# Kernel tuning notes

Measured on AMD Instinct MI355X. Metric: run time of the kernel, lower is better.

The kernel has to match this reference:

```python
import jax, jax.numpy as jnp
import numpy as np

N_NODES = 50000
N_EDGES = 800000
LATENT = 32
NODE_IN = 6
EDGE_IN = 3
STEPS = 10
OUT_DIM = 1
NEG_SLOPE = 0.01
LN_EPS = 1e-5


def _leaky(x):
    return jnp.where(x >= 0, x, NEG_SLOPE * x)


def _layernorm(x, scale, bias):
    mu = jnp.mean(x, axis=-1, keepdims=True)
    var = jnp.mean(jnp.square(x - mu), axis=-1, keepdims=True)
    return (x - mu) * jax.lax.rsqrt(var + LN_EPS) * scale + bias


def setup_inputs() -> dict:
    key = jax.random.key(0)
    ks = jax.random.split(key, 24)
    g = lambda i, shape, fan_in: (jax.random.normal(ks[i], shape, jnp.float32)
                                  / np.sqrt(fan_in)).astype(jnp.float32)
    return {
        "x": jax.random.normal(ks[0], (N_NODES, NODE_IN), jnp.float32),
        "edge_attr": jax.random.normal(ks[1], (N_EDGES, EDGE_IN), jnp.float32),
        "senders": jax.random.randint(ks[2], (N_EDGES,), 0, N_NODES, jnp.int32),
        "receivers": jax.random.randint(ks[3], (N_EDGES,), 0, N_NODES, jnp.int32),
        # input embedders (Linear + LeakyReLU)
        "node_enc_W": g(4, (NODE_IN, LATENT), NODE_IN),
        "node_enc_b": jnp.zeros((LATENT,), jnp.float32),
        "edge_enc_W": g(5, (EDGE_IN, LATENT), EDGE_IN),
        "edge_enc_b": jnp.zeros((LATENT,), jnp.float32),
        # per-step edge update: concat(e, x_src, x_dst) -> latent
        "edge_W": g(6, (STEPS, 3 * LATENT, LATENT), 3 * LATENT),
        "edge_b": jnp.zeros((STEPS, LATENT), jnp.float32),
        "edge_ln_scale": jnp.ones((STEPS, LATENT), jnp.float32),
        "edge_ln_bias": jnp.zeros((STEPS, LATENT), jnp.float32),
        # per-step node update: concat(x, agg) -> latent
        "node_W": g(7, (STEPS, 2 * LATENT, LATENT), 2 * LATENT),
        "node_b": jnp.zeros((STEPS, LATENT), jnp.float32),
        "node_ln_scale": jnp.ones((STEPS, LATENT), jnp.float32),
        "node_ln_bias": jnp.zeros((STEPS, LATENT), jnp.float32),
        # decoder
        "dec_W1": g(8, (LATENT, LATENT), LATENT),
        "dec_b1": jnp.zeros((LATENT,), jnp.float32),
        "dec_W2": g(9, (LATENT, OUT_DIM), LATENT),
        "dec_b2": jnp.zeros((OUT_DIM,), jnp.float32),
    }


def _forward(x, edge_attr, senders, receivers,
             node_enc_W, node_enc_b, edge_enc_W, edge_enc_b,
             edge_W, edge_b, edge_ln_scale, edge_ln_bias,
             node_W, node_b, node_ln_scale, node_ln_bias,
             dec_W1, dec_b1, dec_W2, dec_b2):
    n = x.shape[0]
    # encode raw features into latent space
    h = _leaky(x @ node_enc_W + node_enc_b)            # [N, L]
    e = _leaky(edge_attr @ edge_enc_W + edge_enc_b)    # [E, L]
    # receiver in-degree for scatter-mean (constant across steps)
    cnt = jax.ops.segment_sum(jnp.ones((e.shape[0],), e.dtype), receivers,
                              num_segments=n)
    inv_cnt = (1.0 / jnp.maximum(cnt, 1.0))[:, None]   # [N, 1]

    def step(carry, p):
        h, e = carry
        eW, eb, es, ebi, nW, nb, ns, nbi = p
        # edge update: MLP(concat(e, h_src, h_dst)) + inner LN + residual
        m = jnp.concatenate([e, h[senders], h[receivers]], axis=-1)  # [E, 3L]
        m = _layernorm(_leaky(m @ eW + eb), es, ebi)
        e = e + m
        # node update: scatter-mean over receivers, MLP + inner LN + residual
        agg = jax.ops.segment_sum(e, receivers, num_segments=n) * inv_cnt
        u = jnp.concatenate([h, agg], axis=-1)                       # [N, 2L]
        u = _layernorm(_leaky(u @ nW + nb), ns, nbi)
        h = h + u
        return (h, e), None

    (h, e), _ = jax.lax.scan(step, (h, e),
                             (edge_W, edge_b, edge_ln_scale, edge_ln_bias,
                              node_W, node_b, node_ln_scale, node_ln_bias))
    # decoder: Linear -> LeakyReLU -> Linear
    return _leaky(h @ dec_W1 + dec_b1) @ dec_W2 + dec_b2  # [N, 1]


def reference(x, edge_attr, senders, receivers,
              node_enc_W, node_enc_b, edge_enc_W, edge_enc_b,
              edge_W, edge_b, edge_ln_scale, edge_ln_bias,
              node_W, node_b, node_ln_scale, node_ln_bias,
              dec_W1, dec_b1, dec_W2, dec_b2):
    return _forward(x, edge_attr, senders, receivers,
                    node_enc_W, node_enc_b, edge_enc_W, edge_enc_b,
                    edge_W, edge_b, edge_ln_scale, edge_ln_bias,
                    node_W, node_b, node_ln_scale, node_ln_bias,
                    dec_W1, dec_b1, dec_W2, dec_b2)
```

## Files before the change

### kernel.cpp

```cpp
#include <hip/hip_runtime.h>
#include <hip/hip_bf16.h>

#define N_NODES 50000
#define N_EDGES 800000
#define LATENT 32
#define STEPS 10
#define NEG_SLOPE 0.01f
#define LN_EPS 1e-5f
#define N_TILES (N_EDGES / 16)
#define TPW 8
#define TILES_PER_BLOCK 32
#define SCAN_BLK 256
#define SCAN_NBLK ((N_NODES + SCAN_BLK - 1) / SCAN_BLK)
#define STG_STRIDE 36

typedef __attribute__((ext_vector_type(8))) __bf16 bf16x8;
typedef __attribute__((ext_vector_type(4))) __bf16 bf16x4;
typedef __attribute__((ext_vector_type(4))) float f32x4;

__device__ __forceinline__ float leaky(float x) {
    return x >= 0.0f ? x : NEG_SLOPE * x;
}

__device__ __forceinline__ float4 f4fma(float a, float4 b, float4 c) {
    c.x += a * b.x; c.y += a * b.y; c.z += a * b.z; c.w += a * b.w;
    return c;
}

__device__ __forceinline__ bf16x4 pack4(float4 v) {
    bf16x4 o;
    o[0] = (__bf16)v.x; o[1] = (__bf16)v.y; o[2] = (__bf16)v.z; o[3] = (__bf16)v.w;
    return o;
}


__global__ void encode_nodes_kernel(const float* __restrict__ x,
                                    const float* __restrict__ W,
                                    const float* __restrict__ b,
                                    float* __restrict__ h,
                                    __bf16* __restrict__ hbf) {
    __shared__ __align__(16) float Ws[6 * 32];
    __shared__ __align__(16) float bs[32];
    int tid = threadIdx.x;
    if (tid < 192) Ws[tid] = W[tid];
    if (tid < 32) bs[tid] = b[tid];
    __syncthreads();
    int n = blockIdx.x * blockDim.x + tid;
    if (n >= N_NODES) return;
    float xv[6];
#pragma unroll
    for (int k = 0; k < 6; k++) xv[k] = x[(size_t)n * 6 + k];
    float4 acc[8];
#pragma unroll
    for (int q = 0; q < 8; q++) acc[q] = *(const float4*)&bs[q * 4];
#pragma unroll
    for (int k = 0; k < 6; k++) {
#pragma unroll
        for (int q = 0; q < 8; q++) {
            float4 w = *(const float4*)&Ws[k * 32 + q * 4];
            acc[q] = f4fma(xv[k], w, acc[q]);
        }
    }
#pragma unroll
    for (int q = 0; q < 8; q++) {
        float4 o = acc[q];
        o.x = leaky(o.x); o.y = leaky(o.y); o.z = leaky(o.z); o.w = leaky(o.w);
        *(float4*)&h[(size_t)n * 32 + q * 4] = o;
        *(bf16x4*)&hbf[(size_t)n * 32 + q * 4] = pack4(o);
    }
}


__global__ void count_kernel(const int* __restrict__ recv, int* __restrict__ cnt) {
    int i = blockIdx.x * blockDim.x + threadIdx.x;
    if (i < N_EDGES) atomicAdd(&cnt[recv[i]], 1);
}

__global__ void csr_reduce_kernel(const int* __restrict__ cnt, int* __restrict__ partial) {
    __shared__ int sdata[SCAN_BLK];
    int tid = threadIdx.x;
    int idx = blockIdx.x * SCAN_BLK + tid;
    sdata[tid] = (idx < N_NODES) ? cnt[idx] : 0;
    __syncthreads();
#pragma unroll
    for (int off = SCAN_BLK / 2; off > 0; off >>= 1) {
        if (tid < off) sdata[tid] += sdata[tid + off];
        __syncthreads();
    }
    if (tid == 0) partial[blockIdx.x] = sdata[0];
}

__global__ void csr_scan_partials_kernel(int* __restrict__ partial,
                                         int* __restrict__ row_start) {
    __shared__ int sdata[SCAN_BLK];
    int tid = threadIdx.x;
    int v = (tid < SCAN_NBLK) ? partial[tid] : 0;
    sdata[tid] = v;
    __syncthreads();
#pragma unroll
    for (int off = 1; off < SCAN_BLK; off <<= 1) {
        int t = (tid >= off) ? sdata[tid - off] : 0;
        __syncthreads();
        sdata[tid] += t;
        __syncthreads();
    }
    if (tid < SCAN_NBLK) partial[tid] = sdata[tid] - v;
    if (tid == SCAN_BLK - 1) row_start[N_NODES] = sdata[SCAN_BLK - 1];
}

__global__ void csr_apply_kernel(const int* __restrict__ cnt,
                                 const int* __restrict__ partial,
                                 int* __restrict__ row_start,
                                 int* __restrict__ cursor) {
    __shared__ int sdata[SCAN_BLK];
    int tid = threadIdx.x;
    int idx = blockIdx.x * SCAN_BLK + tid;
    int v = (idx < N_NODES) ? cnt[idx] : 0;
    sdata[tid] = v;
    __syncthreads();
#pragma unroll
    for (int off = 1; off < SCAN_BLK; off <<= 1) {
        int t = (tid >= off) ? sdata[tid - off] : 0;
        __syncthreads();
        sdata[tid] += t;
        __syncthreads();
    }
    if (idx < N_NODES) {
        int out = partial[blockIdx.x] + sdata[tid] - v;
        row_start[idx] = out;
        cursor[idx] = out;
    }
}

__global__ void scatter_encode_kernel(const float* __restrict__ ea,
                                      const int* __restrict__ senders,
                                      const int* __restrict__ receivers,
                                      int* __restrict__ cursor,
                                      const float* __restrict__ W,
                                      const float* __restrict__ b,
                                      __bf16* __restrict__ e,
                                      unsigned int* __restrict__ sr_p) {
    __shared__ __align__(16) float Ws[3 * 32];
    __shared__ __align__(16) float bs[32];
    int tid = threadIdx.x;
    if (tid < 96) Ws[tid] = W[tid];
    if (tid < 32) bs[tid] = b[tid];
    __syncthreads();
    int i = blockIdx.x * blockDim.x + tid;
    if (i >= N_EDGES) return;
    int s = senders[i];
    int r = receivers[i];
    float xv[3];
#pragma unroll
    for (int k = 0; k < 3; k++) xv[k] = ea[(size_t)i * 3 + k];
    int pos = atomicAdd(&cursor[r], 1);
    float4 acc[8];
#pragma unroll
    for (int q = 0; q < 8; q++) acc[q] = *(const float4*)&bs[q * 4];
#pragma unroll
    for (int k = 0; k < 3; k++) {
#pragma unroll
        for (int q = 0; q < 8; q++) {
            float4 w = *(const float4*)&Ws[k * 32 + q * 4];
            acc[q] = f4fma(xv[k], w, acc[q]);
        }
    }
    __bf16* er = e + (size_t)pos * 32;
#pragma unroll
    for (int q = 0; q < 4; q++) {
        float4 lo = acc[2 * q], hi = acc[2 * q + 1];
        bf16x8 v;
        v[0] = (__bf16)leaky(lo.x); v[1] = (__bf16)leaky(lo.y);
        v[2] = (__bf16)leaky(lo.z); v[3] = (__bf16)leaky(lo.w);
        v[4] = (__bf16)leaky(hi.x); v[5] = (__bf16)leaky(hi.y);
        v[6] = (__bf16)leaky(hi.z); v[7] = (__bf16)leaky(hi.w);
        *(bf16x8*)(er + q * 8) = v;
    }
    sr_p[pos] = (unsigned int)s | ((unsigned int)r << 16);
}


__global__ __launch_bounds__(256) void edge_mfma_kernel(
    __bf16* __restrict__ e,
    const __bf16* __restrict__ hbf,
    const unsigned int* __restrict__ srp,
    const float* __restrict__ W,
    const float* __restrict__ bias,
    const float* __restrict__ ln_s,
    const float* __restrict__ ln_b) {
    __shared__ __align__(16) float Ws[96 * 32];
    __shared__ __align__(16) float prm[96];
    __shared__ __align__(16) float stg[4][16 * STG_STRIDE];
    int tid = threadIdx.x;
    {
        const float4* Wg = (const float4*)W;
        float4* Wl = (float4*)Ws;
#pragma unroll
        for (int r = 0; r < 3; r++) Wl[tid + r * 256] = Wg[tid + r * 256];
        if (tid < 32) {
            prm[tid] = bias[tid];
            prm[32 + tid] = ln_s[tid];
            prm[64 + tid] = ln_b[tid];
        }
    }
    __syncthreads();

    const int wave = tid >> 6;
    const int lane = tid & 63;
    const int n_ = lane & 15;
    const int quad = lane >> 4;
    const int rr = lane >> 2;
    const int jj = lane & 3;

    bf16x8 bf[3][2];
#pragma unroll
    for (int kc = 0; kc < 3; kc++)
#pragma unroll
        for (int oh = 0; oh < 2; oh++) {
            bf16x8 f;
#pragma unroll
            for (int j = 0; j < 8; j++)
                f[j] = (__bf16)Ws[(kc * 32 + quad * 8 + j) * 32 + oh * 16 + n_];
            bf[kc][oh] = f;
        }
    float bia0 = prm[n_], bia1 = prm[16 + n_];
    float lns8[8], lnb8[8];
#pragma unroll
    for (int i = 0; i < 8; i++) {
        lns8[i] = prm[32 + jj * 8 + i];
        lnb8[i] = prm[64 + jj * 8 + i];
    }

    int tile0 = blockIdx.x * TILES_PER_BLOCK + wave * TPW;
    int ntiles = min(TPW, N_TILES - tile0);
    if (ntiles <= 0) return;
    float* mystg = stg[wave];
    const int ed0 = tile0 * 16 + n_;

    unsigned int sr0 = srp[ed0];
    bf16x8 aE = *(const bf16x8*)&e[(size_t)ed0 * 32 + quad * 8];
    bf16x8 aS = *(const bf16x8*)&hbf[(size_t)(sr0 & 0xFFFFu) * 32 + quad * 8];
    bf16x8 aR = *(const bf16x8*)&hbf[(size_t)(sr0 >> 16) * 32 + quad * 8];
    bf16x8 old = *(const bf16x8*)&e[(size_t)(tile0 * 16 + rr) * 32 + jj * 8];
    unsigned int sr_n = 0;
    if (ntiles > 1) sr_n = srp[ed0 + 16];

    for (int t = 0; t < ntiles; t++) {
        int e0 = (tile0 + t) * 16;

        f32x4 acc[2] = {{0.f, 0.f, 0.f, 0.f}, {0.f, 0.f, 0.f, 0.f}};
#pragma unroll
        for (int oh = 0; oh < 2; oh++) {
            acc[oh] = __builtin_amdgcn_mfma_f32_16x16x32_bf16(aE, bf[0][oh], acc[oh], 0, 0, 0);
            acc[oh] = __builtin_amdgcn_mfma_f32_16x16x32_bf16(aS, bf[1][oh], acc[oh], 0, 0, 0);
            acc[oh] = __builtin_amdgcn_mfma_f32_16x16x32_bf16(aR, bf[2][oh], acc[oh], 0, 0, 0);
        }

        bf16x8 aE_n = aE, aS_n = aS, aR_n = aR, old_n = old;
        if (t + 1 < ntiles) {
            int edn = ed0 + (t + 1) * 16;
            aE_n = *(const bf16x8*)&e[(size_t)edn * 32 + quad * 8];
            aS_n = *(const bf16x8*)&hbf[(size_t)(sr_n & 0xFFFFu) * 32 + quad * 8];
            aR_n = *(const bf16x8*)&hbf[(size_t)(sr_n >> 16) * 32 + quad * 8];
            old_n = *(const bf16x8*)&e[(size_t)(e0 + 16 + rr) * 32 + jj * 8];
            if (t + 2 < ntiles) sr_n = srp[ed0 + (t + 2) * 16];
        }

#pragma unroll
        for (int oh = 0; oh < 2; oh++)
#pragma unroll
            for (int g = 0; g < 4; g++)
                mystg[(quad * 4 + g) * STG_STRIDE + oh * 16 + n_] =
                    leaky(acc[oh][g] + (oh ? bia1 : bia0));
        __builtin_amdgcn_wave_barrier();

        f32x4 va = *(const f32x4*)&mystg[rr * STG_STRIDE + jj * 8];
        f32x4 vb = *(const f32x4*)&mystg[rr * STG_STRIDE + jj * 8 + 4];
        float s1 = va[0] + va[1] + va[2] + va[3] + vb[0] + vb[1] + vb[2] + vb[3];
        float s2 = va[0]*va[0] + va[1]*va[1] + va[2]*va[2] + va[3]*va[3]
                 + vb[0]*vb[0] + vb[1]*vb[1] + vb[2]*vb[2] + vb[3]*vb[3];
        s1 += __shfl_xor(s1, 1);  s2 += __shfl_xor(s2, 1);
        s1 += __shfl_xor(s1, 2);  s2 += __shfl_xor(s2, 2);
        float mu = s1 * (1.0f / 32.0f);
        float var = s2 * (1.0f / 32.0f) - mu * mu;
        float inv = rsqrtf(fmaxf(var, 0.0f) + LN_EPS);

        float v[8] = {va[0], va[1], va[2], va[3], vb[0], vb[1], vb[2], vb[3]};
        bf16x8 outp;
#pragma unroll
        for (int i = 0; i < 8; i++)
            outp[i] = (__bf16)((float)old[i] + (v[i] - mu) * inv * lns8[i] + lnb8[i]);
        *(bf16x8*)&e[(size_t)(e0 + rr) * 32 + jj * 8] = outp;
        __builtin_amdgcn_wave_barrier();

        aE = aE_n; aS = aS_n; aR = aR_n; old = old_n;
    }
}


__global__ void node_kernel(float* __restrict__ h,
                            __bf16* __restrict__ hbf,
                            const __bf16* __restrict__ e,
                            const int* __restrict__ row_start,
                            const float* __restrict__ W,
                            const float* __restrict__ bias,
                            const float* __restrict__ ln_s,
                            const float* __restrict__ ln_b) {
    __shared__ __align__(16) float Ws[64 * 32];
    __shared__ __align__(16) float prm[96];
    int tid = threadIdx.x;
    {
        const float4* Wg = (const float4*)W;
        float4* Wl = (float4*)Ws;
#pragma unroll
        for (int r = 0; r < 2; r++) Wl[tid + r * 256] = Wg[tid + r * 256];
        if (tid < 32) {
            prm[tid] = bias[tid];
            prm[32 + tid] = ln_s[tid];
            prm[64 + tid] = ln_b[tid];
        }
    }
    __syncthreads();
    int n = blockIdx.x * blockDim.x + tid;
    if (n >= N_NODES) return;

    int beg = row_start[n], end = row_start[n + 1];
    float c[64];
#pragma unroll
    for (int q = 0; q < 8; q++) {
        float4 v = *(const float4*)&h[(size_t)n * 32 + q * 4];
        c[q * 4 + 0] = v.x; c[q * 4 + 1] = v.y; c[q * 4 + 2] = v.z; c[q * 4 + 3] = v.w;
    }
    float s[32];
#pragma unroll
    for (int k = 0; k < 32; k++) s[k] = 0.0f;
    for (int j = beg; j < end; j++) {
        const __bf16* er = e + (size_t)j * 32;
#pragma unroll
        for (int q = 0; q < 4; q++) {
            bf16x8 v = *(const bf16x8*)(er + q * 8);
#pragma unroll
            for (int k = 0; k < 8; k++) s[q * 8 + k] += (float)v[k];
        }
    }
    float ic = 1.0f / fmaxf((float)(end - beg), 1.0f);
#pragma unroll
    for (int k = 0; k < 32; k++) c[32 + k] = s[k] * ic;

    float4 acc[8];
#pragma unroll
    for (int q = 0; q < 8; q++) acc[q] = *(const float4*)&prm[q * 4];
#pragma unroll
    for (int k = 0; k < 64; k++) {
#pragma unroll
        for (int q = 0; q < 8; q++) {
            float4 w = *(const float4*)&Ws[k * 32 + q * 4];
            acc[q] = f4fma(c[k], w, acc[q]);
        }
    }
    float m[32];
#pragma unroll
    for (int q = 0; q < 8; q++) {
        m[q * 4 + 0] = leaky(acc[q].x);
        m[q * 4 + 1] = leaky(acc[q].y);
        m[q * 4 + 2] = leaky(acc[q].z);
        m[q * 4 + 3] = leaky(acc[q].w);
    }
    float s1 = 0.0f, s2 = 0.0f;
#pragma unroll
    for (int i = 0; i < 32; i++) { s1 += m[i]; s2 += m[i] * m[i]; }
    float mu = s1 * (1.0f / 32.0f);
    float var = s2 * (1.0f / 32.0f) - mu * mu;
    float inv = rsqrtf(fmaxf(var, 0.0f) + LN_EPS);
#pragma unroll
    for (int q = 0; q < 8; q++) {
        float4 sc = *(const float4*)&prm[32 + q * 4];
        float4 bi = *(const float4*)&prm[64 + q * 4];
        float4 res;
        res.x = c[q * 4 + 0] + (m[q * 4 + 0] - mu) * inv * sc.x + bi.x;
        res.y = c[q * 4 + 1] + (m[q * 4 + 1] - mu) * inv * sc.y + bi.y;
        res.z = c[q * 4 + 2] + (m[q * 4 + 2] - mu) * inv * sc.z + bi.z;
        res.w = c[q * 4 + 3] + (m[q * 4 + 3] - mu) * inv * sc.w + bi.w;
        *(float4*)&h[(size_t)n * 32 + q * 4] = res;
        *(bf16x4*)&hbf[(size_t)n * 32 + q * 4] = pack4(res);
    }
}


__global__ void decoder_kernel(const float* __restrict__ h,
                               const float* __restrict__ W1,
                               const float* __restrict__ b1,
                               const float* __restrict__ W2,
                               const float* __restrict__ b2,
                               float* __restrict__ out) {
    __shared__ __align__(16) float W1s[32 * 32];
    __shared__ __align__(16) float prm[65];
    int tid = threadIdx.x;
    {
        const float4* Wg = (const float4*)W1;
        float4* Wl = (float4*)W1s;
        Wl[tid] = Wg[tid];
        if (tid < 32) { prm[tid] = b1[tid]; prm[32 + tid] = W2[tid]; }
        if (tid == 0) prm[64] = b2[0];
    }
    __syncthreads();
    int n = blockIdx.x * blockDim.x + tid;
    if (n >= N_NODES) return;
    float hv[32];
#pragma unroll
    for (int q = 0; q < 8; q++) {
        float4 v = *(const float4*)&h[(size_t)n * 32 + q * 4];
        hv[q * 4 + 0] = v.x; hv[q * 4 + 1] = v.y; hv[q * 4 + 2] = v.z; hv[q * 4 + 3] = v.w;
    }
    float4 acc[8];
#pragma unroll
    for (int q = 0; q < 8; q++) acc[q] = *(const float4*)&prm[q * 4];
#pragma unroll
    for (int k = 0; k < 32; k++) {
#pragma unroll
        for (int q = 0; q < 8; q++) {
            float4 w = *(const float4*)&W1s[k * 32 + q * 4];
            acc[q] = f4fma(hv[k], w, acc[q]);
        }
    }
    float o = prm[64];
#pragma unroll
    for (int q = 0; q < 8; q++) {
        o += leaky(acc[q].x) * prm[32 + q * 4 + 0];
        o += leaky(acc[q].y) * prm[32 + q * 4 + 1];
        o += leaky(acc[q].z) * prm[32 + q * 4 + 2];
        o += leaky(acc[q].w) * prm[32 + q * 4 + 3];
    }
    out[n] = o;
}


extern "C" void kernel_launch(void* const* d_in, const int* in_sizes, int n_in,
                              void* d_out, int out_size, void* d_ws, size_t ws_size,
                              hipStream_t stream) {
    const float* x          = (const float*)d_in[0];
    const float* edge_attr  = (const float*)d_in[1];
    const int*   senders    = (const int*)d_in[2];
    const int*   receivers  = (const int*)d_in[3];
    const float* node_enc_W = (const float*)d_in[4];
    const float* node_enc_b = (const float*)d_in[5];
    const float* edge_enc_W = (const float*)d_in[6];
    const float* edge_enc_b = (const float*)d_in[7];
    const float* edge_W     = (const float*)d_in[8];
    const float* edge_b     = (const float*)d_in[9];
    const float* edge_ln_s  = (const float*)d_in[10];
    const float* edge_ln_b  = (const float*)d_in[11];
    const float* node_W     = (const float*)d_in[12];
    const float* node_b     = (const float*)d_in[13];
    const float* node_ln_s  = (const float*)d_in[14];
    const float* node_ln_b  = (const float*)d_in[15];
    const float* dec_W1     = (const float*)d_in[16];
    const float* dec_b1     = (const float*)d_in[17];
    const float* dec_W2     = (const float*)d_in[18];
    const float* dec_b2     = (const float*)d_in[19];
    float* out = (float*)d_out;

    char* ws = (char*)d_ws;
    size_t off = 0;
    auto alloc = [&](size_t bytes) -> void* {
        void* p = ws + off;
        off = (off + bytes + 255) & ~(size_t)255;
        return p;
    };
    float*        h         = (float*)alloc((size_t)N_NODES * 32 * 4);
    __bf16*       hbf       = (__bf16*)alloc((size_t)N_NODES * 32 * 2);
    __bf16*       e         = (__bf16*)alloc((size_t)N_EDGES * 32 * 2);
    int*          cnt       = (int*)alloc((size_t)N_NODES * 4);
    int*          row_start = (int*)alloc((size_t)(N_NODES + 1) * 4);
    int*          cursor    = (int*)alloc((size_t)N_NODES * 4);
    unsigned int* sr_p      = (unsigned int*)alloc((size_t)N_EDGES * 4);
    int*          partial   = (int*)alloc((size_t)SCAN_BLK * 4);
    (void)ws_size; (void)in_sizes; (void)n_in; (void)out_size;

    hipMemsetAsync(cnt, 0, (size_t)N_NODES * 4, stream);
    encode_nodes_kernel<<<(N_NODES + 255) / 256, 256, 0, stream>>>(x, node_enc_W, node_enc_b, h, hbf);
    count_kernel<<<(N_EDGES + 255) / 256, 256, 0, stream>>>(receivers, cnt);
    csr_reduce_kernel<<<SCAN_NBLK, SCAN_BLK, 0, stream>>>(cnt, partial);
    csr_scan_partials_kernel<<<1, SCAN_BLK, 0, stream>>>(partial, row_start);
    csr_apply_kernel<<<SCAN_NBLK, SCAN_BLK, 0, stream>>>(cnt, partial, row_start, cursor);
    scatter_encode_kernel<<<(N_EDGES + 255) / 256, 256, 0, stream>>>(
        edge_attr, senders, receivers, cursor, edge_enc_W, edge_enc_b, e, sr_p);

    int edge_blocks = (N_TILES + TILES_PER_BLOCK - 1) / TILES_PER_BLOCK;
    for (int s = 0; s < STEPS; s++) {
        edge_mfma_kernel<<<edge_blocks, 256, 0, stream>>>(
            e, hbf, sr_p,
            edge_W + (size_t)s * 96 * 32, edge_b + s * 32,
            edge_ln_s + s * 32, edge_ln_b + s * 32);
        node_kernel<<<(N_NODES + 255) / 256, 256, 0, stream>>>(
            h, hbf, e, row_start, node_W + (size_t)s * 64 * 32, node_b + s * 32,
            node_ln_s + s * 32, node_ln_b + s * 32);
    }
    decoder_kernel<<<(N_NODES + 255) / 256, 256, 0, stream>>>(h, dec_W1, dec_b1, dec_W2, dec_b2, out);
}
```

Before: 743.8 us.

## Split node update across two lanes per node with shuffle reduction

Each node is now processed by two adjacent threads, each owning half of the feature columns for the gather and half of the K dimension of the 64x32 matvec. Partial accumulators are combined with a shuffle-xor, and each half writes its own 16 output columns. The intent is more threads in flight, fewer registers per thread, and coalesced half-row edge reads, at the cost of one shuffle reduction and a duplicated LayerNorm computation.

```diff
diff --git a/kernel.cpp b/kernel.cpp
--- a/kernel.cpp
+++ b/kernel.cpp
@@ -321,43 +321,62 @@
         }
     }
     __syncthreads();
-    int n = blockIdx.x * blockDim.x + tid;
+    int g = blockIdx.x * blockDim.x + tid;
+    int n = g >> 1, half = g & 1;
     if (n >= N_NODES) return;
 
     int beg = row_start[n], end = row_start[n + 1];
-    float c[64];
+    float ch[16];
+#pragma unroll
+    for (int q = 0; q < 4; q++) {
+        float4 v = *(const float4*)&h[(size_t)n * 32 + half * 16 + q * 4];
+        ch[q * 4 + 0] = v.x; ch[q * 4 + 1] = v.y; ch[q * 4 + 2] = v.z; ch[q * 4 + 3] = v.w;
+    }
+    float s[16];
+#pragma unroll
+    for (int k = 0; k < 16; k++) s[k] = 0.0f;
+    for (int j = beg; j < end; j++) {
+        const __bf16* er = e + (size_t)j * 32 + half * 16;
+        bf16x8 v0 = *(const bf16x8*)er;
+        bf16x8 v1 = *(const bf16x8*)(er + 8);
+#pragma unroll
+        for (int k = 0; k < 8; k++) { s[k] += (float)v0[k]; s[8 + k] += (float)v1[k]; }
+    }
+    float ic = 1.0f / fmaxf((float)(end - beg), 1.0f);
+    float ca[16];
+#pragma unroll
+    for (int k = 0; k < 16; k++) ca[k] = s[k] * ic;
+
+    float4 acc[8];
+    if (half == 0) {
+#pragma unroll
+        for (int q = 0; q < 8; q++) acc[q] = *(const float4*)&prm[q * 4];
+    } else {
+#pragma unroll
+        for (int q = 0; q < 8; q++) acc[q] = make_float4(0.f, 0.f, 0.f, 0.f);
+    }
+#pragma unroll
+    for (int i = 0; i < 16; i++) {
+        int kh = half * 16 + i;
+#pragma unroll
+        for (int q = 0; q < 8; q++)
+            acc[q] = f4fma(ch[i], *(const float4*)&Ws[kh * 32 + q * 4], acc[q]);
+    }
+#pragma unroll
+    for (int i = 0; i < 16; i++) {
+        int ka = 32 + half * 16 + i;
+#pragma unroll
+        for (int q = 0; q < 8; q++)
+            acc[q] = f4fma(ca[i], *(const float4*)&Ws[ka * 32 + q * 4], acc[q]);
+    }
 #pragma unroll
     for (int q = 0; q < 8; q++) {
-        float4 v = *(const float4*)&h[(size_t)n * 32 + q * 4];
-        c[q * 4 + 0] = v.x; c[q * 4 + 1] = v.y; c[q * 4 + 2] = v.z; c[q * 4 + 3] = v.w;
-    }
-    float s[32];
-#pragma unroll
-    for (int k = 0; k < 32; k++) s[k] = 0.0f;
-    for (int j = beg; j < end; j++) {
-        const __bf16* er = e + (size_t)j * 32;
-#pragma unroll
-        for (int q = 0; q < 4; q++) {
-            bf16x8 v = *(const bf16x8*)(er + q * 8);
-#pragma unroll
-            for (int k = 0; k < 8; k++) s[q * 8 + k] += (float)v[k];
-        }
-    }
-    float ic = 1.0f / fmaxf((float)(end - beg), 1.0f);
-#pragma unroll
-    for (int k = 0; k < 32; k++) c[32 + k] = s[k] * ic;
-
-    float4 acc[8];
-#pragma unroll
-    for (int q = 0; q < 8; q++) acc[q] = *(const float4*)&prm[q * 4];
-#pragma unroll
-    for (int k = 0; k < 64; k++) {
-#pragma unroll
-        for (int q = 0; q < 8; q++) {
-            float4 w = *(const float4*)&Ws[k * 32 + q * 4];
-            acc[q] = f4fma(c[k], w, acc[q]);
-        }
-    }
+        acc[q].x += __shfl_xor(acc[q].x, 1);
+        acc[q].y += __shfl_xor(acc[q].y, 1);
+        acc[q].z += __shfl_xor(acc[q].z, 1);
+        acc[q].w += __shfl_xor(acc[q].w, 1);
+    }
+
     float m[32];
 #pragma unroll
     for (int q = 0; q < 8; q++) {
@@ -372,18 +391,26 @@
     float mu = s1 * (1.0f / 32.0f);
     float var = s2 * (1.0f / 32.0f) - mu * mu;
     float inv = rsqrtf(fmaxf(var, 0.0f) + LN_EPS);
-#pragma unroll
-    for (int q = 0; q < 8; q++) {
-        float4 sc = *(const float4*)&prm[32 + q * 4];
-        float4 bi = *(const float4*)&prm[64 + q * 4];
+
+    bf16x8 hb0, hb1;
+#pragma unroll
+    for (int q = 0; q < 4; q++) {
+        int col = half * 16 + q * 4;
+        float4 sc = *(const float4*)&prm[32 + col];
+        float4 bi = *(const float4*)&prm[64 + col];
         float4 res;
-        res.x = c[q * 4 + 0] + (m[q * 4 + 0] - mu) * inv * sc.x + bi.x;
-        res.y = c[q * 4 + 1] + (m[q * 4 + 1] - mu) * inv * sc.y + bi.y;
-        res.z = c[q * 4 + 2] + (m[q * 4 + 2] - mu) * inv * sc.z + bi.z;
-        res.w = c[q * 4 + 3] + (m[q * 4 + 3] - mu) * inv * sc.w + bi.w;
-        *(float4*)&h[(size_t)n * 32 + q * 4] = res;
-        *(bf16x4*)&hbf[(size_t)n * 32 + q * 4] = pack4(res);
-    }
+        res.x = ch[q * 4 + 0] + (m[col + 0] - mu) * inv * sc.x + bi.x;
+        res.y = ch[q * 4 + 1] + (m[col + 1] - mu) * inv * sc.y + bi.y;
+        res.z = ch[q * 4 + 2] + (m[col + 2] - mu) * inv * sc.z + bi.z;
+        res.w = ch[q * 4 + 3] + (m[col + 3] - mu) * inv * sc.w + bi.w;
+        *(float4*)&h[(size_t)n * 32 + col] = res;
+        bf16x8& dst = (q < 2) ? hb0 : hb1;
+        int base = (q & 1) * 4;
+        dst[base + 0] = (__bf16)res.x; dst[base + 1] = (__bf16)res.y;
+        dst[base + 2] = (__bf16)res.z; dst[base + 3] = (__bf16)res.w;
+    }
+    *(bf16x8*)&hbf[(size_t)n * 32 + half * 16] = hb0;
+    *(bf16x8*)&hbf[(size_t)n * 32 + half * 16 + 8] = hb1;
 }
 
 
@@ -492,7 +519,7 @@
             e, hbf, sr_p,
             edge_W + (size_t)s * 96 * 32, edge_b + s * 32,
             edge_ln_s + s * 32, edge_ln_b + s * 32);
-        node_kernel<<<(N_NODES + 255) / 256, 256, 0, stream>>>(
+        node_kernel<<<(2 * N_NODES + 255) / 256, 256, 0, stream>>>(
             h, hbf, e, row_start, node_W + (size_t)s * 64 * 32, node_b + s * 32,
             node_ln_s + s * 32, node_ln_b + s * 32);
     }
```

New measurement: 759.3 us. 2.1% more time.
